# Kernel optimization log

Hardware: AMD Instinct MI355X
Metric: run time of the kernel (lower is better)

## Reference

```python
import jax, jax.numpy as jnp
import numpy as np

K = 64          # number of tags, incl. BOS/EOS
V = 50000       # vocab size (excl. BOS/EOS words)
D = 128         # lexicon embedding dim
BOS_T = K - 2   # BOS tag index
EOS_T = K - 1   # EOS tag index
BATCH = 8192
L = 126         # interior words per sentence (n = L + 2 incl. BOS/EOS)
EPS = 1e-45     # smoothing added to A and B in updateAB


def setup_inputs() -> dict:
    key = jax.random.key(0)
    k1, k2, k3, k4 = jax.random.split(key, 4)
    words = jax.random.randint(k1, (BATCH, L), 0, V, dtype=jnp.int32)
    ThetaB = 0.01 * jax.random.uniform(k2, (K, D), dtype=jnp.float32)
    WA = 0.01 * jax.random.uniform(k3, (K, K), dtype=jnp.float32)
    E = jax.random.normal(k4, (V, D), dtype=jnp.float32)
    return {"words": words, "ThetaB": ThetaB, "WA": WA, "E": E}


def reference(words, ThetaB, WA, E):
    # updateAB(): A = softmax(WA) with BOS column forced to prob 0 (-inf logit)
    WAm = WA.at[:, BOS_T].set(-jnp.inf)
    A = jax.nn.softmax(WAm, axis=1) + EPS                       # [K, K]
    B = jax.nn.softmax(ThetaB @ E.T, axis=1)                    # [K, V]
    B = B.at[EOS_T, :].set(0.0).at[BOS_T, :].set(0.0) + EPS
    logA = jnp.log(A)                                           # [K, K]
    logB = jnp.log(B)                                           # [K, V]

    # Emission log-probs gathered per token: [L, B, K]
    em = jnp.swapaxes(logB.T[words], 0, 1)

    # alpha_0: one-hot (in log space) at BOS tag
    alpha0 = jnp.full((words.shape[0], K), -jnp.inf, dtype=logA.dtype)
    alpha0 = alpha0.at[:, BOS_T].set(0.0)

    def step(alpha, e):
        # alpha: [B, K] over prev tags; logsumexp over prev tag axis
        new = jax.nn.logsumexp(alpha[:, :, None] + logA[None, :, :], axis=1) + e
        return new, None

    alpha, _ = jax.lax.scan(step, alpha0, em)
    # Final transition into EOS tag (no emission): log Z per sentence, [B]
    logZ = jax.nn.logsumexp(alpha + logA[None, :, EOS_T], axis=1)
    return logZ
```

## Files before the change

### kernel.cpp

```cpp
#include <hip/hip_runtime.h>
#include <hip/hip_bf16.h>
#include <math.h>


#define KT 64
#define VV 50000
#define DD 128
#define BOS_T 62
#define EOS_T 63
#define LLEN 126
#define EPSF 1e-45f
#define SCALE_F 65536.0f
#define LOG_TOTAL_SCALE (2016.0f * 0.6931471805599453f)
#define PITCH 68
#define NBLK 782
#define PBLK 784

#define BTN_OFF   0
#define A_OFF     6400000
#define SUM_OFF   6416384
#define PART_OFF  6416640

typedef short short8 __attribute__((ext_vector_type(8)));
typedef float f32x4  __attribute__((ext_vector_type(4)));

union U8 { short8 v; unsigned u[4]; short s[8]; };

static __device__ inline unsigned short f2bf_u(float x) {
    __hip_bfloat16 h = __float2bfloat16(x);
    return *reinterpret_cast<unsigned short*>(&h);
}
static __device__ inline short f2bf(float x) { return (short)f2bf_u(x); }
static __device__ inline unsigned pk2(float a, float b) {
    return (unsigned)f2bf_u(a) | ((unsigned)f2bf_u(b) << 16);
}
static __device__ inline float lo16(unsigned u) { union { unsigned i; float f; } c; c.i = u << 16;        return c.f; }
static __device__ inline float hi16(unsigned u) { union { unsigned i; float f; } c; c.i = u & 0xffff0000u; return c.f; }

__global__ __launch_bounds__(64) void k_prepA(const float* __restrict__ WA,
                                              float* __restrict__ A) {
    int i = blockIdx.x;
    int j = threadIdx.x;
    float wv = WA[i * KT + j];
    float e = (j == BOS_T) ? 0.0f : __expf(wv);
    float s = e;
#pragma unroll
    for (int off = 32; off > 0; off >>= 1) s += __shfl_xor(s, off, 64);
    A[i * KT + j] = e / s + EPSF;
}

__global__ __launch_bounds__(256) void k_emit(const float* __restrict__ ThetaB,
                                              const float* __restrict__ E,
                                              unsigned short* __restrict__ btn_bf,
                                              float* __restrict__ partial) {
    __shared__ float red[4][KT];
    int t    = threadIdx.x;
    int lane = t & 63;
    int w    = t >> 6;
    int n    = lane & 15;
    int q    = lane >> 4;
    int v0   = (blockIdx.x * 4 + w) * 16;

    short8 Bf[4][4];
#pragma unroll
    for (int kt = 0; kt < 4; ++kt)
#pragma unroll
        for (int nt = 0; nt < 4; ++nt) {
            const float* p = ThetaB + (nt * 16 + n) * DD + kt * 32 + q * 8;
            float4 x = *(const float4*)p;
            float4 y = *(const float4*)(p + 4);
            U8 f;
            f.u[0] = pk2(x.x, x.y); f.u[1] = pk2(x.z, x.w);
            f.u[2] = pk2(y.x, y.y); f.u[3] = pk2(y.z, y.w);
            Bf[kt][nt] = f.v;
        }

    int rowE = v0 + n; rowE = rowE < VV ? rowE : VV - 1;
    short8 Ae[4];
#pragma unroll
    for (int kt = 0; kt < 4; ++kt) {
        const float* p = E + (size_t)rowE * DD + kt * 32 + q * 8;
        float4 x = *(const float4*)p;
        float4 y = *(const float4*)(p + 4);
        U8 f;
        f.u[0] = pk2(x.x, x.y); f.u[1] = pk2(x.z, x.w);
        f.u[2] = pk2(y.x, y.y); f.u[3] = pk2(y.z, y.w);
        Ae[kt] = f.v;
    }

#pragma unroll
    for (int nt = 0; nt < 4; ++nt) {
        f32x4 C = {0.f, 0.f, 0.f, 0.f};
#pragma unroll
        for (int kt = 0; kt < 4; ++kt)
            C = __builtin_amdgcn_mfma_f32_16x16x32_bf16(Ae[kt], Bf[kt][nt], C, 0, 0, 0);
        float ps = 0.0f;
#pragma unroll
        for (int r = 0; r < 4; ++r) {
            int row = v0 + 4 * q + r;
            float e = __expf(C[r]);
            if (row < VV) {
                btn_bf[(size_t)row * KT + nt * 16 + n] = f2bf_u(e);
                ps += e;
            }
        }
        ps += __shfl_xor(ps, 16, 64);
        ps += __shfl_xor(ps, 32, 64);
        if (q == 0) red[w][nt * 16 + n] = ps;
    }
    __syncthreads();
    if (w == 0) {
        float s = red[0][lane] + red[1][lane] + red[2][lane] + red[3][lane];
        partial[lane * PBLK + blockIdx.x] = s;
    }
}

__global__ __launch_bounds__(256) void k_sum(const float* __restrict__ partial,
                                             float* __restrict__ sumexp) {
    __shared__ float r[4];
    int k = blockIdx.x;
    int t = threadIdx.x;
    float s = 0.0f;
    for (int i = t; i < NBLK; i += 256) s += partial[k * PBLK + i];
#pragma unroll
    for (int off = 32; off > 0; off >>= 1) s += __shfl_xor(s, off, 64);
    if ((t & 63) == 0) r[t >> 6] = s;
    __syncthreads();
    if (t == 0) sumexp[k] = r[0] + r[1] + r[2] + r[3];
}

__global__ __launch_bounds__(256) void k_norm(unsigned short* __restrict__ btn_bf,
                                              const float* __restrict__ sumexp) {
    __shared__ float rs[KT];
    int t = threadIdx.x;
    if (t < KT) {
        float s = sumexp[t];
        rs[t] = (t == BOS_T || t == EOS_T) ? 0.0f : (SCALE_F / s);
    }
    __syncthreads();
    uint4* b4 = (uint4*)btn_bf;
    const int n8 = VV * KT / 8;
    int i = blockIdx.x * 256 + t;
    if (i < n8) {
        uint4 x = b4[i];
        int k0 = (i & 7) * 8;
        unsigned r0 = pk2(lo16(x.x) * rs[k0 + 0], hi16(x.x) * rs[k0 + 1]);
        unsigned r1 = pk2(lo16(x.y) * rs[k0 + 2], hi16(x.y) * rs[k0 + 3]);
        unsigned r2 = pk2(lo16(x.z) * rs[k0 + 4], hi16(x.z) * rs[k0 + 5]);
        unsigned r3 = pk2(lo16(x.w) * rs[k0 + 6], hi16(x.w) * rs[k0 + 7]);
        b4[i] = make_uint4(r0, r1, r2, r3);
    }
}

__global__ __launch_bounds__(64) void k_fwd(const int* __restrict__ words,
                                            const unsigned short* __restrict__ btn_bf,
                                            const float* __restrict__ A,
                                            float* __restrict__ out) {
    __shared__ __attribute__((aligned(16))) float sh[16 * PITCH];
    int lane = threadIdx.x & 63;
    int n    = lane & 15;
    int q    = lane >> 4;
    int b0   = blockIdx.x * 16;

    short8 Bf[2][4];
#pragma unroll
    for (int kt = 0; kt < 2; ++kt)
#pragma unroll
        for (int nt = 0; nt < 4; ++nt) {
            U8 f;
#pragma unroll
            for (int j = 0; j < 8; ++j)
                f.s[j] = f2bf(A[(kt * 32 + q * 8 + j) * KT + nt * 16 + n]);
            Bf[kt][nt] = f.v;
        }
    short8 Bfin[2];
#pragma unroll
    for (int kt = 0; kt < 2; ++kt) {
        U8 f;
#pragma unroll
        for (int j = 0; j < 8; ++j)
            f.s[j] = (n == 0) ? f2bf(A[(kt * 32 + q * 8 + j) * KT + EOS_T]) : (short)0;
        Bfin[kt] = f.v;
    }

    U8 a0, a1;
#pragma unroll
    for (int j = 0; j < 4; ++j) { a0.u[j] = 0; a1.u[j] = 0; }
    if (q == 3) a1.s[6] = (short)0x3F80;
    short8 Af0 = a0.v, Af1 = a1.v;

    const int* wrow = words + (size_t)(b0 + n) * LLEN;

    int wa = wrow[0], wb = wrow[1], wc = wrow[2];
    uint4 e0a = *(const uint4*)(btn_bf + (size_t)wa * KT + q * 8);
    uint4 e1a = *(const uint4*)(btn_bf + (size_t)wa * KT + 32 + q * 8);
    uint4 e0b = *(const uint4*)(btn_bf + (size_t)wb * KT + q * 8);
    uint4 e1b = *(const uint4*)(btn_bf + (size_t)wb * KT + 32 + q * 8);
    uint4 e0c = *(const uint4*)(btn_bf + (size_t)wc * KT + q * 8);
    uint4 e1c = *(const uint4*)(btn_bf + (size_t)wc * KT + 32 + q * 8);
    int wn = wrow[3];

    for (int l = 0; l < LLEN; ++l) {
        uint4 e0d = *(const uint4*)(btn_bf + (size_t)wn * KT + q * 8);
        uint4 e1d = *(const uint4*)(btn_bf + (size_t)wn * KT + 32 + q * 8);
        int wi = l + 4; wi = wi < LLEN ? wi : LLEN - 1;
        wn = wrow[wi];

        f32x4 C[4];
#pragma unroll
        for (int nt = 0; nt < 4; ++nt) {
            f32x4 acc = {0.f, 0.f, 0.f, 0.f};
            acc = __builtin_amdgcn_mfma_f32_16x16x32_bf16(Af0, Bf[0][nt], acc, 0, 0, 0);
            acc = __builtin_amdgcn_mfma_f32_16x16x32_bf16(Af1, Bf[1][nt], acc, 0, 0, 0);
            C[nt] = acc;
        }

#pragma unroll
        for (int nt = 0; nt < 4; ++nt)
#pragma unroll
            for (int r = 0; r < 4; ++r)
                sh[(4 * q + r) * PITCH + nt * 16 + n] = C[nt][r];
        asm volatile("s_waitcnt lgkmcnt(0)" ::: "memory");

        {
            const float* p = sh + n * PITCH + q * 8;
            float4 lo = *(const float4*)p;
            float4 hi = *(const float4*)(p + 4);
            U8 f;
            f.u[0] = pk2(lo.x * lo16(e0a.x), lo.y * hi16(e0a.x));
            f.u[1] = pk2(lo.z * lo16(e0a.y), lo.w * hi16(e0a.y));
            f.u[2] = pk2(hi.x * lo16(e0a.z), hi.y * hi16(e0a.z));
            f.u[3] = pk2(hi.z * lo16(e0a.w), hi.w * hi16(e0a.w));
            Af0 = f.v;
        }
        {
            const float* p = sh + n * PITCH + 32 + q * 8;
            float4 lo = *(const float4*)p;
            float4 hi = *(const float4*)(p + 4);
            U8 f;
            f.u[0] = pk2(lo.x * lo16(e1a.x), lo.y * hi16(e1a.x));
            f.u[1] = pk2(lo.z * lo16(e1a.y), lo.w * hi16(e1a.y));
            f.u[2] = pk2(hi.x * lo16(e1a.z), hi.y * hi16(e1a.z));
            f.u[3] = pk2(hi.z * lo16(e1a.w), hi.w * hi16(e1a.w));
            Af1 = f.v;
        }
        e0a = e0b; e1a = e1b;
        e0b = e0c; e1b = e1c;
        e0c = e0d; e1c = e1d;
    }

    f32x4 Cf = {0.f, 0.f, 0.f, 0.f};
    Cf = __builtin_amdgcn_mfma_f32_16x16x32_bf16(Af0, Bfin[0], Cf, 0, 0, 0);
    Cf = __builtin_amdgcn_mfma_f32_16x16x32_bf16(Af1, Bfin[1], Cf, 0, 0, 0);
    if (n == 0) {
#pragma unroll
        for (int r = 0; r < 4; ++r)
            out[b0 + 4 * q + r] = logf(Cf[r]) - LOG_TOTAL_SCALE;
    }
}

extern "C" void kernel_launch(void* const* d_in, const int* in_sizes, int n_in,
                              void* d_out, int out_size, void* d_ws, size_t ws_size,
                              hipStream_t stream) {
    const int*   words  = (const int*)d_in[0];
    const float* ThetaB = (const float*)d_in[1];
    const float* WA     = (const float*)d_in[2];
    const float* E      = (const float*)d_in[3];
    float* out = (float*)d_out;

    char* ws = (char*)d_ws;
    unsigned short* btn_bf = (unsigned short*)(ws + BTN_OFF);
    float* A       = (float*)(ws + A_OFF);
    float* sumexp  = (float*)(ws + SUM_OFF);
    float* partial = (float*)(ws + PART_OFF);

    k_prepA<<<64, 64, 0, stream>>>(WA, A);
    k_emit<<<NBLK, 256, 0, stream>>>(ThetaB, E, btn_bf, partial);
    k_sum<<<KT, 256, 0, stream>>>(partial, sumexp);
    k_norm<<<(VV * KT / 8 + 255) / 256, 256, 0, stream>>>(btn_bf, sumexp);
    k_fwd<<<8192 / 16, 64, 0, stream>>>(words, btn_bf, A, out);
}
```

Before: 152.5 us.

## Fold emission normalization into transition matrix, drop k_norm, use packed bf16 convert

Removes the separate k_norm pass over the 50000x64 bf16 emission table. The per-tag normalization scale is folded into the columns of the transition matrix inside k_fwd, which is algebraically equivalent because the scale applies per destination tag. Several other changes ride along: pk2 uses the hardware packed bf16 conversion builtin when available, k_emit issues its E loads before converting ThetaB, the forward loop is unrolled by 3, and the LDS waitcnt is replaced by wave barriers. Risks include bf16 rounding now being applied to unnormalized emissions, and possibly incorrect LDS ordering if the compiler-inserted waits do not cover the removed explicit waitcnt.

```diff
diff --git a/kernel.cpp b/kernel.cpp
--- a/kernel.cpp
+++ b/kernel.cpp
@@ -31,9 +31,20 @@
     return *reinterpret_cast<unsigned short*>(&h);
 }
 static __device__ inline short f2bf(float x) { return (short)f2bf_u(x); }
+
+#if __has_builtin(__builtin_amdgcn_cvt_pk_bf16_f32)
+typedef __bf16 bf16x2 __attribute__((ext_vector_type(2)));
 static __device__ inline unsigned pk2(float a, float b) {
-    return (unsigned)f2bf_u(a) | ((unsigned)f2bf_u(b) << 16);
-}
+    bf16x2 r = __builtin_amdgcn_cvt_pk_bf16_f32(a, b);
+    return *reinterpret_cast<unsigned*>(&r);
+}
+#else
+static __device__ inline unsigned pk2(float a, float b) {
+    union { float f; unsigned u; } ua, ub;
+    ua.f = a; ub.f = b;
+    return ((ua.u + 0x8000u) >> 16) | ((ub.u + 0x8000u) & 0xFFFF0000u);
+}
+#endif
 static __device__ inline float lo16(unsigned u) { union { unsigned i; float f; } c; c.i = u << 16;        return c.f; }
 static __device__ inline float hi16(unsigned u) { union { unsigned i; float f; } c; c.i = u & 0xffff0000u; return c.f; }
 
@@ -61,6 +72,15 @@
     int q    = lane >> 4;
     int v0   = (blockIdx.x * 4 + w) * 16;
 
+    int rowE = v0 + n; rowE = rowE < VV ? rowE : VV - 1;
+    float4 ex[4][2];
+#pragma unroll
+    for (int kt = 0; kt < 4; ++kt) {
+        const float* p = E + (size_t)rowE * DD + kt * 32 + q * 8;
+        ex[kt][0] = *(const float4*)p;
+        ex[kt][1] = *(const float4*)(p + 4);
+    }
+
     short8 Bf[4][4];
 #pragma unroll
     for (int kt = 0; kt < 4; ++kt)
@@ -75,16 +95,12 @@
             Bf[kt][nt] = f.v;
         }
 
-    int rowE = v0 + n; rowE = rowE < VV ? rowE : VV - 1;
     short8 Ae[4];
 #pragma unroll
     for (int kt = 0; kt < 4; ++kt) {
-        const float* p = E + (size_t)rowE * DD + kt * 32 + q * 8;
-        float4 x = *(const float4*)p;
-        float4 y = *(const float4*)(p + 4);
         U8 f;
-        f.u[0] = pk2(x.x, x.y); f.u[1] = pk2(x.z, x.w);
-        f.u[2] = pk2(y.x, y.y); f.u[3] = pk2(y.z, y.w);
+        f.u[0] = pk2(ex[kt][0].x, ex[kt][0].y); f.u[1] = pk2(ex[kt][0].z, ex[kt][0].w);
+        f.u[2] = pk2(ex[kt][1].x, ex[kt][1].y); f.u[3] = pk2(ex[kt][1].z, ex[kt][1].w);
         Ae[kt] = f.v;
     }
 
@@ -129,32 +145,10 @@
     if (t == 0) sumexp[k] = r[0] + r[1] + r[2] + r[3];
 }
 
-__global__ __launch_bounds__(256) void k_norm(unsigned short* __restrict__ btn_bf,
-                                              const float* __restrict__ sumexp) {
-    __shared__ float rs[KT];
-    int t = threadIdx.x;
-    if (t < KT) {
-        float s = sumexp[t];
-        rs[t] = (t == BOS_T || t == EOS_T) ? 0.0f : (SCALE_F / s);
-    }
-    __syncthreads();
-    uint4* b4 = (uint4*)btn_bf;
-    const int n8 = VV * KT / 8;
-    int i = blockIdx.x * 256 + t;
-    if (i < n8) {
-        uint4 x = b4[i];
-        int k0 = (i & 7) * 8;
-        unsigned r0 = pk2(lo16(x.x) * rs[k0 + 0], hi16(x.x) * rs[k0 + 1]);
-        unsigned r1 = pk2(lo16(x.y) * rs[k0 + 2], hi16(x.y) * rs[k0 + 3]);
-        unsigned r2 = pk2(lo16(x.z) * rs[k0 + 4], hi16(x.z) * rs[k0 + 5]);
-        unsigned r3 = pk2(lo16(x.w) * rs[k0 + 6], hi16(x.w) * rs[k0 + 7]);
-        b4[i] = make_uint4(r0, r1, r2, r3);
-    }
-}
-
 __global__ __launch_bounds__(64) void k_fwd(const int* __restrict__ words,
                                             const unsigned short* __restrict__ btn_bf,
                                             const float* __restrict__ A,
+                                            const float* __restrict__ sumexp,
                                             float* __restrict__ out) {
     __shared__ __attribute__((aligned(16))) float sh[16 * PITCH];
     int lane = threadIdx.x & 63;
@@ -162,6 +156,14 @@
     int q    = lane >> 4;
     int b0   = blockIdx.x * 16;
 
+    float rs4[4];
+#pragma unroll
+    for (int nt = 0; nt < 4; ++nt) {
+        int col = nt * 16 + n;
+        float s = sumexp[col];
+        rs4[nt] = (col == BOS_T || col == EOS_T) ? 0.0f : (SCALE_F / s);
+    }
+
     short8 Bf[2][4];
 #pragma unroll
     for (int kt = 0; kt < 2; ++kt)
@@ -170,7 +172,7 @@
             U8 f;
 #pragma unroll
             for (int j = 0; j < 8; ++j)
-                f.s[j] = f2bf(A[(kt * 32 + q * 8 + j) * KT + nt * 16 + n]);
+                f.s[j] = f2bf(A[(kt * 32 + q * 8 + j) * KT + nt * 16 + n] * rs4[nt]);
             Bf[kt][nt] = f.v;
         }
     short8 Bfin[2];
@@ -200,6 +202,7 @@
     uint4 e1c = *(const uint4*)(btn_bf + (size_t)wc * KT + 32 + q * 8);
     int wn = wrow[3];
 
+#pragma unroll 3
     for (int l = 0; l < LLEN; ++l) {
         uint4 e0d = *(const uint4*)(btn_bf + (size_t)wn * KT + q * 8);
         uint4 e1d = *(const uint4*)(btn_bf + (size_t)wn * KT + 32 + q * 8);
@@ -220,7 +223,7 @@
 #pragma unroll
             for (int r = 0; r < 4; ++r)
                 sh[(4 * q + r) * PITCH + nt * 16 + n] = C[nt][r];
-        asm volatile("s_waitcnt lgkmcnt(0)" ::: "memory");
+        __builtin_amdgcn_wave_barrier();
 
         {
             const float* p = sh + n * PITCH + q * 8;
@@ -244,6 +247,7 @@
             f.u[3] = pk2(hi.z * lo16(e1a.w), hi.w * hi16(e1a.w));
             Af1 = f.v;
         }
+        __builtin_amdgcn_wave_barrier();
         e0a = e0b; e1a = e1b;
         e0b = e0c; e1b = e1c;
         e0c = e0d; e1c = e1d;
@@ -277,6 +281,5 @@
     k_prepA<<<64, 64, 0, stream>>>(WA, A);
     k_emit<<<NBLK, 256, 0, stream>>>(ThetaB, E, btn_bf, partial);
     k_sum<<<KT, 256, 0, stream>>>(partial, sumexp);
-    k_norm<<<(VV * KT / 8 + 255) / 256, 256, 0, stream>>>(btn_bf, sumexp);
-    k_fwd<<<8192 / 16, 64, 0, stream>>>(words, btn_bf, A, out);
-}
+    k_fwd<<<8192 / 16, 64, 0, stream>>>(words, btn_bf, A, sumexp, out);
+}
```

New measurement: 170.2 us. 11.6% more time.
